# Optimization experiments

Hardware: AMD Instinct MI355X
Metric: run time of the kernel (lower is better)

Reference implementation:

```python
import jax, jax.numpy as jnp
import numpy as np

B, S, D, OUT = 8, 4096, 2048, 2048
M = 128          # number of saved edit masks
TOP_K = 256
IRR_THRESHOLD = 0.3


def setup_inputs() -> dict:
    key = jax.random.key(0)
    ks = jax.random.split(key, 8)
    x = jax.random.normal(ks[0], (B, S, D), dtype=jnp.float32)
    boundaries = jax.random.randint(ks[1], (B,), 128, S, dtype=jnp.int64)
    weight = jax.random.normal(ks[2], (OUT, D), dtype=jnp.float32) * 0.02
    bias = jax.random.normal(ks[3], (OUT,), dtype=jnp.float32) * 0.02
    new_weight = jax.random.normal(ks[4], (OUT, D), dtype=jnp.float32) * 0.02
    permutation = jax.random.permutation(ks[5], D).astype(jnp.int64)
    # saved masks: exactly TOP_K active dims per stored edit
    scores = jax.random.normal(ks[6], (M, D), dtype=jnp.float32)
    _, idx = jax.lax.top_k(scores, TOP_K)
    saved_masks = jnp.zeros((M, D), dtype=jnp.bool_).at[
        jnp.arange(M)[:, None], idx].set(True)
    bg_mean = jax.random.normal(ks[7], (D,), dtype=jnp.float32) * 0.02
    return {
        "x": x, "boundaries": boundaries, "weight": weight, "bias": bias,
        "new_weight": new_weight, "permutation": permutation,
        "saved_masks": saved_masks, "bg_mean": bg_mean, "top_k": TOP_K,
    }


def reference(x, boundaries, weight, bias, new_weight, permutation,
              saved_masks, bg_mean, top_k):
    bsz, seq_len, dim = x.shape
    # --- aggregate prompt features: masked mean up to boundary, decentered ---
    b = jnp.clip(boundaries, 0, seq_len - 1)
    pos = jnp.arange(seq_len)[None, :]                     # [1, S]
    pmask = (pos <= b[:, None]).astype(x.dtype)            # [B, S]
    denom = jnp.maximum(pmask.sum(axis=1, keepdims=True), 1.0)
    prompt_agg = jnp.einsum('bsd,bs->bd', x, pmask) / denom
    prompt_agg = prompt_agg - bg_mean[None, :]             # mean_decentered
    # --- TopHasher: top-k of |features|, then permute indices ---
    _, top_idx = jax.lax.top_k(jnp.abs(prompt_agg), top_k)  # [B, K]
    active_indices = permutation[top_idx]                   # [B, K]
    active_mask = jnp.zeros((bsz, dim), dtype=jnp.bool_).at[
        jnp.arange(bsz)[:, None], active_indices].set(True)
    # --- retrieve best-overlapping saved mask ---
    overlap = active_mask.astype(jnp.float32) @ saved_masks.T.astype(jnp.float32)
    overlap_ratios = overlap / float(top_k)                 # [B, M]
    best_idx = jnp.argmax(overlap_ratios, axis=1)
    best_overlap = jnp.max(overlap_ratios, axis=1)
    relevant = best_overlap >= IRR_THRESHOLD                # [B]
    best_masks = saved_masks[best_idx]                      # [B, D]
    final_mask = jnp.where(relevant[:, None], best_masks,
                           jnp.zeros_like(best_masks))
    # --- masked new-weight path + original linear ---
    x_hashed = x * final_mask.astype(x.dtype)[:, None, :]
    new_out = jnp.einsum('bsd,od->bso', x_hashed, new_weight)
    orig_out = jnp.einsum('bsd,od->bso', x, weight) + bias
    return orig_out + new_out
```

## Files before the change

### kernel.cpp

```cpp
#include <hip/hip_runtime.h>
#include <stdint.h>

typedef unsigned short u16;
typedef __attribute__((ext_vector_type(4))) float f32x4;
typedef __attribute__((ext_vector_type(8))) u16 u16x8;
typedef __attribute__((ext_vector_type(8))) __bf16 bf16x8;

#define B_ 8
#define S_ 4096
#define D_ 2048
#define O_ 2048
#define M_ 128
#define KTOP_ 256

__device__ __forceinline__ u16 f2bf(float f) {
  unsigned int u = __float_as_uint(f);
  u = (u + 0x7FFFu + ((u >> 16) & 1u)) >> 16;
  return (u16)u;
}

__device__ __forceinline__ void g2l16(const void* g, void* l) {
  __builtin_amdgcn_global_load_lds(
      (const __attribute__((address_space(1))) unsigned int*)g,
      (__attribute__((address_space(3))) unsigned int*)l,
      16, 0, 0);
}

__global__ __launch_bounds__(256) void cvt_bf16(const float* __restrict__ x,
                                                u16* __restrict__ xb) {
  int64_t idx = (int64_t)blockIdx.x * 256 + threadIdx.x;
  int64_t e = idx * 8;
  f32x4 a = *(const f32x4*)(x + e);
  f32x4 b = *(const f32x4*)(x + e + 4);
  u16x8 r;
  r[0] = f2bf(a[0]); r[1] = f2bf(a[1]); r[2] = f2bf(a[2]); r[3] = f2bf(a[3]);
  r[4] = f2bf(b[0]); r[5] = f2bf(b[1]); r[6] = f2bf(b[2]); r[7] = f2bf(b[3]);
  *(u16x8*)(xb + e) = r;
}

__global__ __launch_bounds__(256) void prompt_sums(const float* __restrict__ x,
                                                   const int* __restrict__ boundaries,
                                                   float* __restrict__ sums) {
  const int b = blockIdx.z, dt = blockIdx.x, sc = blockIdx.y;
  const int d = dt * 256 + threadIdx.x;
  int bclip = min(max(boundaries[b], 0), S_ - 1);
  const int chunk = S_ / 16;
  int s0 = sc * chunk;
  int s1 = min(s0 + chunk, bclip + 1);
  if (s1 <= s0) return;
  const float* xp = x + (size_t)b * S_ * D_ + (size_t)s0 * D_ + d;
  float acc = 0.f;
  for (int s = s0; s < s1; ++s, xp += D_) acc += *xp;
  atomicAdd(&sums[b * D_ + d], acc);
}

__global__ __launch_bounds__(512) void topk_mask(const float* __restrict__ sums,
                                                 const int* __restrict__ boundaries,
                                                 const float* __restrict__ bg_mean,
                                                 const int* __restrict__ perm,
                                                 unsigned char* __restrict__ active) {
  const int b = blockIdx.x;
  __shared__ float v[D_];
  int bclip = min(max(boundaries[b], 0), S_ - 1);
  float denom = fmaxf((float)(bclip + 1), 1.0f);
  for (int d = threadIdx.x; d < D_; d += 512)
    v[d] = fabsf(sums[b * D_ + d] / denom - bg_mean[d]);
  __syncthreads();
  for (int d = threadIdx.x; d < D_; d += 512) {
    float my = v[d];
    int cnt = 0;
    for (int j = 0; j < D_; ++j) {
      float o = v[j];
      cnt += (o > my) || (o == my && j < d);
    }
    if (cnt < KTOP_) active[b * D_ + perm[d]] = 1;
  }
}

__global__ __launch_bounds__(128) void select_mask(const unsigned char* __restrict__ active,
                                                   const unsigned char* __restrict__ saved,
                                                   unsigned char* __restrict__ final_mask) {
  const int b = blockIdx.x;
  const int m = threadIdx.x;
  __shared__ __align__(16) unsigned char act[D_];
  __shared__ int cnts[M_];
  __shared__ int sh_best, sh_rel;
  for (int d = m; d < D_; d += 128) act[d] = active[b * D_ + d];
  __syncthreads();
  const unsigned int* sp = (const unsigned int*)(saved + (size_t)m * D_);
  const unsigned int* ap = (const unsigned int*)act;
  int c = 0;
  for (int i = 0; i < D_ / 4; ++i) c += __popc(sp[i] & ap[i]);
  cnts[m] = c;
  __syncthreads();
  if (m == 0) {
    int best = cnts[0], bi = 0;
    for (int i = 1; i < M_; ++i)
      if (cnts[i] > best) { best = cnts[i]; bi = i; }
    sh_best = bi;
    sh_rel = (best >= 77) ? 1 : 0;
  }
  __syncthreads();
  int bi = sh_best, rel = sh_rel;
  for (int d = m; d < D_; d += 128)
    final_mask[b * D_ + d] = rel ? saved[(size_t)bi * D_ + d] : 0;
}

__global__ __launch_bounds__(256) void build_weff(const float* __restrict__ w,
                                                  const float* __restrict__ nw,
                                                  const unsigned char* __restrict__ fmask,
                                                  u16* __restrict__ weff) {
  int idx = blockIdx.x * 256 + threadIdx.x;
  int bb = idx >> 19;
  int rem = (idx & 524287) << 3;
  int d = rem & (D_ - 1);
  f32x4 w0 = *(const f32x4*)(w + rem);
  f32x4 w1 = *(const f32x4*)(w + rem + 4);
  f32x4 n0 = *(const f32x4*)(nw + rem);
  f32x4 n1 = *(const f32x4*)(nw + rem + 4);
  const unsigned char* mp = fmask + bb * D_ + d;
  u16x8 r;
#pragma unroll
  for (int i = 0; i < 4; ++i) r[i] = f2bf(w0[i] + (mp[i] ? n0[i] : 0.f));
#pragma unroll
  for (int i = 0; i < 4; ++i) r[4 + i] = f2bf(w1[i] + (mp[4 + i] ? n1[i] : 0.f));
  *(u16x8*)(weff + ((size_t)bb << 22) + rem) = r;
}

__global__ __launch_bounds__(256) void gemm_bt(const u16* __restrict__ X,
                                               const u16* __restrict__ W,
                                               const float* __restrict__ bias,
                                               float* __restrict__ out) {
  __shared__ __align__(16) u16 lA[128 * 32];
  __shared__ __align__(16) u16 lB[128 * 32];
  const int b = blockIdx.z, mt = blockIdx.y, nt = blockIdx.x;
  const int t = threadIdx.x;
  const int wave = t >> 6, lane = t & 63;
  const int wr = (wave >> 1) * 64, wc = (wave & 1) * 64;
  const int q = lane >> 4, lm = lane & 15;

  const u16* Ab = X + (size_t)b * S_ * D_ + (size_t)(mt * 128) * D_;
  const u16* Bb = W + (size_t)b * O_ * D_ + (size_t)(nt * 128) * D_;

  const int r0 = t >> 2;
  const int c0 = (t & 3) * 8;

  f32x4 acc[4][4] = {};

  for (int k0 = 0; k0 < D_; k0 += 32) {
    g2l16(Ab + (size_t)r0 * D_ + k0 + c0, lA + t * 8);
    g2l16(Ab + (size_t)(r0 + 64) * D_ + k0 + c0, lA + (t + 256) * 8);
    g2l16(Bb + (size_t)r0 * D_ + k0 + c0, lB + t * 8);
    g2l16(Bb + (size_t)(r0 + 64) * D_ + k0 + c0, lB + (t + 256) * 8);
    __syncthreads();

    bf16x8 af[4], bf[4];
#pragma unroll
    for (int i = 0; i < 4; ++i)
      af[i] = *(const bf16x8*)(lA + (wr + i * 16 + lm) * 32 + q * 8);
#pragma unroll
    for (int j = 0; j < 4; ++j)
      bf[j] = *(const bf16x8*)(lB + (wc + j * 16 + lm) * 32 + q * 8);
#pragma unroll
    for (int i = 0; i < 4; ++i)
#pragma unroll
      for (int j = 0; j < 4; ++j)
        acc[i][j] = __builtin_amdgcn_mfma_f32_16x16x32_bf16(af[i], bf[j], acc[i][j], 0, 0, 0);
    __syncthreads();
  }

  const int col0 = nt * 128 + wc + lm;
  const int row0 = mt * 128 + wr + q * 4;
  float bv[4];
#pragma unroll
  for (int j = 0; j < 4; ++j) bv[j] = bias[col0 + j * 16];
#pragma unroll
  for (int i = 0; i < 4; ++i) {
#pragma unroll
    for (int r = 0; r < 4; ++r) {
      const int row = row0 + i * 16 + r;
      float* op = out + (size_t)b * S_ * O_ + (size_t)row * O_;
#pragma unroll
      for (int j = 0; j < 4; ++j) op[col0 + j * 16] = acc[i][j][r] + bv[j];
    }
  }
}

extern "C" void kernel_launch(void* const* d_in, const int* in_sizes, int n_in,
                              void* d_out, int out_size, void* d_ws, size_t ws_size,
                              hipStream_t stream) {
  const float* x          = (const float*)d_in[0];
  const int* boundaries   = (const int*)d_in[1];
  const float* weight     = (const float*)d_in[2];
  const float* bias       = (const float*)d_in[3];
  const float* new_weight = (const float*)d_in[4];
  const int* perm         = (const int*)d_in[5];
  const unsigned char* saved = (const unsigned char*)d_in[6];
  const float* bg_mean    = (const float*)d_in[7];
  float* out = (float*)d_out;

  char* ws = (char*)d_ws;
  const size_t off_xb   = 0;
  const size_t off_weff = off_xb + (size_t)B_ * S_ * D_ * 2;
  const size_t off_sums = off_weff + (size_t)B_ * O_ * D_ * 2;
  const size_t off_act  = off_sums + (size_t)B_ * D_ * 4;
  const size_t off_fin  = off_act + (size_t)B_ * D_;

  u16* xb   = (u16*)(ws + off_xb);
  u16* weff = (u16*)(ws + off_weff);
  float* sums = (float*)(ws + off_sums);
  unsigned char* act = (unsigned char*)(ws + off_act);
  unsigned char* fin = (unsigned char*)(ws + off_fin);

  hipMemsetAsync(ws + off_sums, 0, (size_t)B_ * D_ * 4 + (size_t)B_ * D_, stream);

  cvt_bf16<<<(B_ * S_ * D_ / 8) / 256, 256, 0, stream>>>(x, xb);
  prompt_sums<<<dim3(D_ / 256, 16, B_), 256, 0, stream>>>(x, boundaries, sums);
  topk_mask<<<B_, 512, 0, stream>>>(sums, boundaries, bg_mean, perm, act);
  select_mask<<<B_, 128, 0, stream>>>(act, saved, fin);
  build_weff<<<(B_ * O_ * D_ / 8) / 256, 256, 0, stream>>>(weight, new_weight, fin, weff);
  gemm_bt<<<dim3(O_ / 128, S_ / 128, B_), 256, 0, stream>>>(xb, weff, bias, out);
}
```

Measured before the change: 1.182 ms.

## Fuse bf16 conversion with prompt sums, radix-select top-k, swizzle GEMM tiles

Merges the x-to-bf16 conversion and the masked prompt-sum reduction into one pass over x, so the 256 MB input is read once instead of up to twice. Replaces the O(D^2) rank-counting top-k with a 4-pass byte radix select over float bits, with a serial tie-break over equal values. Also remaps the GEMM grid to a 1D launch that interleaves batches and groups tiles 4x4 for better L2 reuse. The fused kernel uses fewer, longer-running blocks with 4-wide accesses, and the serial tie loop adds a small single-thread cost.

```diff
diff --git a/kernel.cpp b/kernel.cpp
--- a/kernel.cpp
+++ b/kernel.cpp
@@ -3,6 +3,7 @@
 
 typedef unsigned short u16;
 typedef __attribute__((ext_vector_type(4))) float f32x4;
+typedef __attribute__((ext_vector_type(4))) u16 u16x4;
 typedef __attribute__((ext_vector_type(8))) u16 u16x8;
 typedef __attribute__((ext_vector_type(8))) __bf16 bf16x8;
 
@@ -26,54 +27,82 @@
       16, 0, 0);
 }
 
-__global__ __launch_bounds__(256) void cvt_bf16(const float* __restrict__ x,
-                                                u16* __restrict__ xb) {
-  int64_t idx = (int64_t)blockIdx.x * 256 + threadIdx.x;
-  int64_t e = idx * 8;
-  f32x4 a = *(const f32x4*)(x + e);
-  f32x4 b = *(const f32x4*)(x + e + 4);
-  u16x8 r;
-  r[0] = f2bf(a[0]); r[1] = f2bf(a[1]); r[2] = f2bf(a[2]); r[3] = f2bf(a[3]);
-  r[4] = f2bf(b[0]); r[5] = f2bf(b[1]); r[6] = f2bf(b[2]); r[7] = f2bf(b[3]);
-  *(u16x8*)(xb + e) = r;
-}
-
-__global__ __launch_bounds__(256) void prompt_sums(const float* __restrict__ x,
-                                                   const int* __restrict__ boundaries,
+__global__ __launch_bounds__(256) void cvt_and_sum(const float* __restrict__ x,
+                                                   const int* __restrict__ bnd,
+                                                   u16* __restrict__ xb,
                                                    float* __restrict__ sums) {
-  const int b = blockIdx.z, dt = blockIdx.x, sc = blockIdx.y;
-  const int d = dt * 256 + threadIdx.x;
-  int bclip = min(max(boundaries[b], 0), S_ - 1);
-  const int chunk = S_ / 16;
-  int s0 = sc * chunk;
-  int s1 = min(s0 + chunk, bclip + 1);
-  if (s1 <= s0) return;
+  const int b = blockIdx.z;
+  const int s0 = blockIdx.y * 64;
+  const int d = blockIdx.x * 1024 + threadIdx.x * 4;
+  const int bclip = min(max(bnd[b], 0), S_ - 1);
   const float* xp = x + (size_t)b * S_ * D_ + (size_t)s0 * D_ + d;
-  float acc = 0.f;
-  for (int s = s0; s < s1; ++s, xp += D_) acc += *xp;
-  atomicAdd(&sums[b * D_ + d], acc);
-}
-
-__global__ __launch_bounds__(512) void topk_mask(const float* __restrict__ sums,
-                                                 const int* __restrict__ boundaries,
+  u16* op = xb + (size_t)b * S_ * D_ + (size_t)s0 * D_ + d;
+  const int smax = min(64, bclip + 1 - s0);
+  float a0 = 0.f, a1 = 0.f, a2 = 0.f, a3 = 0.f;
+  for (int i = 0; i < 64; ++i) {
+    f32x4 v = *(const f32x4*)xp;
+    u16x4 r;
+    r[0] = f2bf(v[0]); r[1] = f2bf(v[1]); r[2] = f2bf(v[2]); r[3] = f2bf(v[3]);
+    *(u16x4*)op = r;
+    if (i < smax) { a0 += v[0]; a1 += v[1]; a2 += v[2]; a3 += v[3]; }
+    xp += D_; op += D_;
+  }
+  if (smax > 0) {
+    atomicAdd(&sums[b * D_ + d + 0], a0);
+    atomicAdd(&sums[b * D_ + d + 1], a1);
+    atomicAdd(&sums[b * D_ + d + 2], a2);
+    atomicAdd(&sums[b * D_ + d + 3], a3);
+  }
+}
+
+__global__ __launch_bounds__(256) void topk_mask(const float* __restrict__ sums,
+                                                 const int* __restrict__ bnd,
                                                  const float* __restrict__ bg_mean,
                                                  const int* __restrict__ perm,
                                                  unsigned char* __restrict__ active) {
   const int b = blockIdx.x;
-  __shared__ float v[D_];
-  int bclip = min(max(boundaries[b], 0), S_ - 1);
-  float denom = fmaxf((float)(bclip + 1), 1.0f);
-  for (int d = threadIdx.x; d < D_; d += 512)
-    v[d] = fabsf(sums[b * D_ + d] / denom - bg_mean[d]);
-  __syncthreads();
-  for (int d = threadIdx.x; d < D_; d += 512) {
-    float my = v[d];
-    int cnt = 0;
-    for (int j = 0; j < D_; ++j) {
-      float o = v[j];
-      cnt += (o > my) || (o == my && j < d);
+  __shared__ unsigned int vb[D_];
+  __shared__ int hist[256];
+  __shared__ int sh_sel, sh_cum;
+  const int bclip = min(max(bnd[b], 0), S_ - 1);
+  const float denom = (float)(bclip + 1);
+  for (int d = threadIdx.x; d < D_; d += 256) {
+    float v = fabsf(sums[b * D_ + d] / denom - bg_mean[d]);
+    vb[d] = __float_as_uint(v);
+  }
+  __syncthreads();
+  unsigned int prefix = 0;
+  int r = KTOP_;
+  for (int byte = 3; byte >= 0; --byte) {
+    for (int i = threadIdx.x; i < 256; i += 256) hist[i] = 0;
+    __syncthreads();
+    const unsigned int shift = byte * 8;
+    const unsigned int pmask = (byte == 3) ? 0u : (0xFFFFFFFFu << (shift + 8));
+    for (int d = threadIdx.x; d < D_; d += 256) {
+      unsigned int v = vb[d];
+      if ((v & pmask) == prefix) atomicAdd(&hist[(v >> shift) & 0xFF], 1);
     }
-    if (cnt < KTOP_) active[b * D_ + perm[d]] = 1;
+    __syncthreads();
+    if (threadIdx.x == 0) {
+      int cum = 0, sel = 0;
+      for (int v = 255; v >= 0; --v) {
+        if (cum + hist[v] >= r) { sel = v; break; }
+        cum += hist[v];
+      }
+      sh_sel = sel; sh_cum = cum;
+    }
+    __syncthreads();
+    prefix |= ((unsigned int)sh_sel) << shift;
+    r -= sh_cum;
+    __syncthreads();
+  }
+  const unsigned int T = prefix;
+  for (int d = threadIdx.x; d < D_; d += 256)
+    if (vb[d] > T) active[b * D_ + perm[d]] = 1;
+  if (threadIdx.x == 0) {
+    int need = r;
+    for (int d = 0; d < D_ && need > 0; ++d)
+      if (vb[d] == T) { active[b * D_ + perm[d]] = 1; --need; }
   }
 }
 
@@ -101,7 +130,7 @@
     sh_rel = (best >= 77) ? 1 : 0;
   }
   __syncthreads();
-  int bi = sh_best, rel = sh_rel;
+  const int bi = sh_best, rel = sh_rel;
   for (int d = m; d < D_; d += 128)
     final_mask[b * D_ + d] = rel ? saved[(size_t)bi * D_ + d] : 0;
 }
@@ -133,25 +162,30 @@
                                                float* __restrict__ out) {
   __shared__ __align__(16) u16 lA[128 * 32];
   __shared__ __align__(16) u16 lB[128 * 32];
-  const int b = blockIdx.z, mt = blockIdx.y, nt = blockIdx.x;
-  const int t = threadIdx.x;
-  const int wave = t >> 6, lane = t & 63;
+  const unsigned int gid = blockIdx.x;
+  const int b = gid & 7;
+  const int t = gid >> 3;
+  const int st = t >> 4, wi = t & 15;
+  const int mt = (st & 7) * 4 + (wi & 3);
+  const int nt = (st >> 3) * 4 + (wi >> 2);
+  const int tid = threadIdx.x;
+  const int wave = tid >> 6, lane = tid & 63;
   const int wr = (wave >> 1) * 64, wc = (wave & 1) * 64;
   const int q = lane >> 4, lm = lane & 15;
 
   const u16* Ab = X + (size_t)b * S_ * D_ + (size_t)(mt * 128) * D_;
   const u16* Bb = W + (size_t)b * O_ * D_ + (size_t)(nt * 128) * D_;
 
-  const int r0 = t >> 2;
-  const int c0 = (t & 3) * 8;
+  const int r0 = tid >> 2;
+  const int c0 = (tid & 3) * 8;
 
   f32x4 acc[4][4] = {};
 
   for (int k0 = 0; k0 < D_; k0 += 32) {
-    g2l16(Ab + (size_t)r0 * D_ + k0 + c0, lA + t * 8);
-    g2l16(Ab + (size_t)(r0 + 64) * D_ + k0 + c0, lA + (t + 256) * 8);
-    g2l16(Bb + (size_t)r0 * D_ + k0 + c0, lB + t * 8);
-    g2l16(Bb + (size_t)(r0 + 64) * D_ + k0 + c0, lB + (t + 256) * 8);
+    g2l16(Ab + (size_t)r0 * D_ + k0 + c0, lA + tid * 8);
+    g2l16(Ab + (size_t)(r0 + 64) * D_ + k0 + c0, lA + (tid + 256) * 8);
+    g2l16(Bb + (size_t)r0 * D_ + k0 + c0, lB + tid * 8);
+    g2l16(Bb + (size_t)(r0 + 64) * D_ + k0 + c0, lB + (tid + 256) * 8);
     __syncthreads();
 
     bf16x8 af[4], bf[4];
@@ -214,10 +248,9 @@
 
   hipMemsetAsync(ws + off_sums, 0, (size_t)B_ * D_ * 4 + (size_t)B_ * D_, stream);
 
-  cvt_bf16<<<(B_ * S_ * D_ / 8) / 256, 256, 0, stream>>>(x, xb);
-  prompt_sums<<<dim3(D_ / 256, 16, B_), 256, 0, stream>>>(x, boundaries, sums);
-  topk_mask<<<B_, 512, 0, stream>>>(sums, boundaries, bg_mean, perm, act);
+  cvt_and_sum<<<dim3(D_ / 1024, S_ / 64, B_), 256, 0, stream>>>(x, boundaries, xb, sums);
+  topk_mask<<<B_, 256, 0, stream>>>(sums, boundaries, bg_mean, perm, act);
   select_mask<<<B_, 128, 0, stream>>>(act, saved, fin);
   build_weff<<<(B_ * O_ * D_ / 8) / 256, 256, 0, stream>>>(weight, new_weight, fin, weff);
-  gemm_bt<<<dim3(O_ / 128, S_ / 128, B_), 256, 0, stream>>>(xb, weff, bias, out);
-}
+  gemm_bt<<<B_ * 512, 256, 0, stream>>>(xb, weff, bias, out);
+}
```

Measured after the change: 1.099 ms. 1.08x faster.
